# Kernel tuning notes

Measured on AMD Instinct MI355X. Metric: run time of the kernel, lower is better.

The kernel has to match this reference:

```python
import jax, jax.numpy as jnp
import numpy as np

PERIOD = 15          # hardcoded in the torch module's forward: STL(series, 15)
N_SEASONAL = 7       # statsmodels STL default seasonal smoother length
N_TREND = 29         # smallest odd >= 1.5*p/(1-1.5/7) = 28.64 -> 29 (statsmodels default)
N_LOWPASS = 17       # smallest odd > period (statsmodels default)
N_INNER = 2          # statsmodels: robust=False -> 2 inner iterations, 0 outer


def _loess_matrix(n, q, ts):
    """Dense linear operator for degree-1 LOESS smoothing of a length-n series
    evaluated at (possibly out-of-range) integer positions ts. Non-robust LOESS is
    linear in y, so smoothing == matmul with this constant matrix."""
    M = np.zeros((len(ts), n), dtype=np.float64)
    qq = min(q, n)
    for i, t in enumerate(ts):
        left = int(np.clip(t - (q - 1) // 2, 0, n - qq))
        right = left + qq - 1
        h = max(t - left, right - t)
        if q > n:
            h += (q - n) / 2.0
        xs = np.arange(left, right + 1, dtype=np.float64)
        w = np.clip(1.0 - (np.abs(xs - t) / h) ** 3, 0.0, None) ** 3  # tricube
        w = w / w.sum()
        xbar = (w * xs).sum()
        var = (w * (xs - xbar) ** 2).sum()
        a = w.copy()
        if var > 1e-12:  # degree-1 local linear fit; fall back to deg-0 if degenerate
            a = w * (1.0 + (t - xbar) * (xs - xbar) / var)
        M[i, left:right + 1] = a
    return M.astype(np.float32)


def _ma(x, k):
    """Moving average of window k along last axis (valid mode)."""
    cs = jnp.cumsum(x, axis=-1)
    cs = jnp.concatenate([jnp.zeros(x.shape[:-1] + (1,), x.dtype), cs], axis=-1)
    return (cs[..., k:] - cs[..., :-k]) / k


def setup_inputs() -> dict:
    key = jax.random.key(0)
    x = jax.random.normal(key, (128, 480, 256), dtype=jnp.float32)  # [B, T, C]
    return {"x": x}


def reference(x):
    B, T, Cc = x.shape
    p = PERIOD
    n_sub = T // p  # cycle-subseries length; T chosen divisible by period

    # Constant LOESS smoothing operators (numpy, baked in as jit constants)
    M_seas = jnp.asarray(_loess_matrix(n_sub, N_SEASONAL, np.arange(-1, n_sub + 1)))  # (n_sub+2, n_sub)
    M_lp = jnp.asarray(_loess_matrix(T, N_LOWPASS, np.arange(T)))                     # (T, T)
    M_trend = jnp.asarray(_loess_matrix(T, N_TREND, np.arange(T)))                    # (T, T)

    y = jnp.transpose(x, (0, 2, 1))  # [B, C, T]
    trend = jnp.zeros_like(y)
    seasonal = jnp.zeros_like(y)

    for _ in range(N_INNER):  # STL inner loop (Cleveland 1990, non-robust)
        # 1. detrend
        D = y - trend
        # 2. cycle-subseries LOESS smoothing, extended one period each side
        Dsub = D.reshape(B, Cc, n_sub, p)                      # subseries along axis 2
        Cext = jnp.einsum('sn,bcnp->bcsp', M_seas, Dsub)       # [B,C,n_sub+2,p]
        Cext = Cext.reshape(B, Cc, (n_sub + 2) * p)            # time order, length T+2p
        # 3. low-pass: MA(p) x2, MA(3), then LOESS(n_l)
        lp = _ma(_ma(_ma(Cext, p), p), 3)                      # length T
        L = jnp.einsum('tn,bcn->bct', M_lp, lp)
        # 4. seasonal = smoothed subseries (center T) minus low-pass
        seasonal = Cext[..., p:p + T] - L
        # 5+6. deseasonalize and trend LOESS
        trend = jnp.einsum('tn,bcn->bct', M_trend, y - seasonal)

    resid = y - seasonal - trend
    seas_plus_resid = jnp.transpose(seasonal + resid, (0, 2, 1))  # [B, T, C]
    trend_out = jnp.transpose(trend, (0, 2, 1))
    return (seas_plus_resid, trend_out)
```

## Files before the change

kernel.cpp:

```cpp
#include <hip/hip_runtime.h>
#include <hip/hip_bf16.h>
#include <stdint.h>

#define TLEN 480
#define NB 128
#define NC 256

typedef short bf16x8 __attribute__((ext_vector_type(8)));
typedef float f32x4 __attribute__((ext_vector_type(4)));
typedef unsigned int u32x4 __attribute__((ext_vector_type(4)));
typedef unsigned short u16;
typedef unsigned int u32;

__device__ inline u16 f2bf(float f) {
    union { float f; uint32_t u; } v; v.f = f;
    uint32_t u = v.u;
    return (u16)((u + 0x7fffu + ((u >> 16) & 1u)) >> 16);
}

__device__ inline u32 pack2bf(float lo, float hi) {
    return __builtin_amdgcn_perm(__float_as_uint(hi), __float_as_uint(lo), 0x07060302u);
}

template<int N, int Q>
__device__ __forceinline__ int loess_wT(int t, float* out) {
    int left = t - (Q - 1) / 2;
    if (left < 0) left = 0;
    if (left > N - Q) left = N - Q;
    int right = left + Q - 1;
    int h = (t - left) > (right - t) ? (t - left) : (right - t);
    double w[Q];
    double wsum = 0.0;
    #pragma unroll
    for (int i = 0; i < Q; ++i) {
        double dist = fabs((double)(left + i - t)) / (double)h;
        double u = 1.0 - dist * dist * dist;
        if (u < 0.0) u = 0.0;
        double wv = u * u * u;
        w[i] = wv; wsum += wv;
    }
    #pragma unroll
    for (int i = 0; i < Q; ++i) w[i] /= wsum;
    double xbar = 0.0;
    #pragma unroll
    for (int i = 0; i < Q; ++i) xbar += w[i] * (double)(left + i);
    double var = 0.0;
    #pragma unroll
    for (int i = 0; i < Q; ++i) { double d = (double)(left + i) - xbar; var += w[i] * d * d; }
    if (var > 1e-12) {
        double tb = (double)t - xbar;
        #pragma unroll
        for (int i = 0; i < Q; ++i) {
            double d = (double)(left + i) - xbar;
            out[i] = (float)(w[i] * (1.0 + tb * d / var));
        }
    } else {
        #pragma unroll
        for (int i = 0; i < Q; ++i) out[i] = (float)w[i];
    }
    return left;
}

__global__ void k_loess(float* Ms, float* w3, float* MlpC, float* MtC) {
    int gid = blockIdx.x * 256 + threadIdx.x;
    if (gid < 34) {
        float wl[7];
        int left = loess_wT<32, 7>(gid - 1, wl);
        float* row = Ms + gid * 32;
        #pragma unroll
        for (int i = 0; i < 32; ++i) row[i] = 0.0f;
        #pragma unroll
        for (int i = 0; i < 7; ++i) row[left + i] = wl[i];
    } else if (gid < 514) {
        int t = gid - 34;
        float wl[17];
        loess_wT<TLEN, 17>(t, wl);
        #pragma unroll
        for (int i = 0; i < 17; ++i) MlpC[t * 17 + i] = wl[i];
    } else if (gid < 994) {
        int t = gid - 514;
        float wl[29];
        loess_wT<TLEN, 29>(t, wl);
        #pragma unroll
        for (int i = 0; i < 29; ++i) MtC[t * 29 + i] = wl[i];
    } else if (gid < 1025) {
        int d = gid - 994;
        int cnt = 0;
        for (int c = 0; c < 3; ++c)
            for (int a = 0; a < 15; ++a) {
                int b = d - a - c;
                if (b >= 0 && b < 15) cnt++;
            }
        w3[d] = (float)((double)cnt / 675.0);
    }
}

__global__ __launch_bounds__(256, 2)
void k_T(const float* __restrict__ x, u16* __restrict__ xT) {
    __shared__ u16 Xs[64 * 488];
    int b = blockIdx.x;
    int cz = blockIdx.y * 64;
    int tid = threadIdx.x;
    int wq = tid & 15, kkq = tid >> 4;
    const float* xp0 = x + (size_t)b * TLEN * NC + (size_t)(kkq * 4) * NC + cz + wq * 4;
    u32* l32 = (u32*)Xs;
    int lbase = (wq * 4) * 244 + kkq * 2;

    float4 ra[4], rb[4];
    #pragma unroll
    for (int q = 0; q < 4; ++q) ra[q] = *(const float4*)(xp0 + q * NC);
    #pragma unroll
    for (int p = 0; p < 8; ++p) {
        float4* cur = (p & 1) ? rb : ra;
        float4* nxt = (p & 1) ? ra : rb;
        if (p < 7) {
            if (p + 1 < 7 || kkq < 8) {
                const float* xp = xp0 + (size_t)(p + 1) * 64 * NC;
                #pragma unroll
                for (int q = 0; q < 4; ++q) nxt[q] = *(const float4*)(xp + q * NC);
            }
        }
        if (p < 7 || kkq < 8) {
            const float* fl = (const float*)cur;
            int o = lbase + p * 32;
            #pragma unroll
            for (int cc = 0; cc < 4; ++cc) {
                uint2 w;
                w.x = pack2bf(fl[0 * 4 + cc], fl[1 * 4 + cc]);
                w.y = pack2bf(fl[2 * 4 + cc], fl[3 * 4 + cc]);
                *(uint2*)(l32 + o + cc * 244) = w;
            }
        }
    }
    __syncthreads();

    u16* dst = xT + ((size_t)b * NC + cz) * TLEN;
    #pragma unroll
    for (int v = 0; v < 15; ++v) {
        int id = v * 256 + tid;
        int c = id / 60, j = id - c * 60;
        *(u32x4*)(dst + (size_t)c * TLEN + j * 8) = *(const u32x4*)&Xs[c * 488 + j * 8];
    }
}

__global__ void k_S(const float* __restrict__ Ms, const float* __restrict__ w3,
                    const float* __restrict__ MlpC, float* __restrict__ S) {
    int id = blockIdx.x * 256 + threadIdx.x;
    if (id >= TLEN * TLEN) return;
    int t = id / TLEN, u = id - t * TLEN;
    int nu = u / 15, ju = u - nu * 15;
    int slp = t - 8;
    if (slp < 0) slp = 0;
    if (slp > TLEN - 17) slp = TLEN - 17;
    float acc = 0.0f;
    for (int k = 0; k < 17; ++k) {
        int i = slp + k;
        int s_lo = (i - ju + 14) / 15;
        float g = 0.0f;
        #pragma unroll
        for (int ds = 0; ds < 3; ++ds) {
            int s = s_lo + ds;
            int d = s * 15 + ju - i;
            if (s >= 0 && s < 34 && d >= 0 && d <= 30)
                g += Ms[s * 32 + nu] * w3[d];
        }
        acc += MlpC[t * 17 + k] * g;
    }
    float val = -acc;
    if (t % 15 == ju) val += Ms[(1 + t / 15) * 32 + nu];
    S[id] = val;
}

__global__ void k_VU(const float* __restrict__ MtC, const float* __restrict__ S,
                     float* __restrict__ U, float* __restrict__ V) {
    int id = blockIdx.x * 256 + threadIdx.x;
    if (id >= TLEN * TLEN) return;
    int t = id / TLEN, u = id - t * TLEN;
    int st = t - 14;
    if (st < 0) st = 0;
    if (st > TLEN - 29) st = TLEN - 29;
    float acc = 0.0f;
    for (int k = 0; k < 29; ++k)
        acc += MtC[t * 29 + k] * S[(size_t)(st + k) * TLEN + u];
    float mt = (u >= st && u < st + 29) ? MtC[t * 29 + (u - st)] : 0.0f;
    V[id] = acc;
    U[id] = mt - acc;
}

__global__ void k_A(const float* __restrict__ U, const float* __restrict__ V,
                    u16* __restrict__ Abf) {
    __shared__ float Vs[16][17];
    __shared__ float Us[16][17];
    int tx = threadIdx.x, ty = threadIdx.y;
    int u = blockIdx.x * 16 + tx;
    int t = blockIdx.y * 16 + ty;
    float acc = 0.0f;
    for (int kt = 0; kt < 30; ++kt) {
        Vs[ty][tx] = V[(size_t)t * TLEN + kt * 16 + tx];
        Us[ty][tx] = U[(size_t)(kt * 16 + ty) * TLEN + u];
        __syncthreads();
        #pragma unroll
        for (int e = 0; e < 16; ++e) acc += Vs[ty][e] * Us[e][tx];
        __syncthreads();
    }
    Abf[(size_t)t * TLEN + u] = f2bf(U[(size_t)t * TLEN + u] + acc);
}

__global__ __launch_bounds__(256, 3)
void k_gemm(const u16* __restrict__ A, const u16* __restrict__ xT,
            const float* __restrict__ x,
            float* __restrict__ out0, float* __restrict__ out1) {
    __shared__ float T[96 * 68];
    int b = blockIdx.x;
    int t0 = blockIdx.y * 96;
    int cz = blockIdx.z * 64;
    int tid = threadIdx.x;
    int wave = tid >> 6, lane = tid & 63;
    int lane15 = lane & 15, quad = lane >> 4;
    int wc = wave & 1, wt = wave >> 1;

    const u16* ap0 = xT + ((size_t)b * NC + cz + wc * 32 + lane15) * TLEN + quad * 8;
    const u16* bp0 = A + (size_t)(t0 + wt * 48 + lane15) * TLEN + quad * 8;

    f32x4 acc[2][3] = {};
    bf16x8 acur[2], anxt[2], bcur[3], bnxt[3];
    acur[0] = *(const bf16x8*)ap0;
    acur[1] = *(const bf16x8*)(ap0 + 16 * TLEN);
    #pragma unroll
    for (int j = 0; j < 3; ++j) bcur[j] = *(const bf16x8*)(bp0 + (size_t)j * 16 * TLEN);

    #pragma unroll
    for (int s = 0; s < 15; ++s) {
        bf16x8* ac = (s & 1) ? anxt : acur;
        bf16x8* an = (s & 1) ? acur : anxt;
        bf16x8* bc = (s & 1) ? bnxt : bcur;
        bf16x8* bn = (s & 1) ? bcur : bnxt;
        if (s < 14) {
            int k = (s + 1) * 32;
            an[0] = *(const bf16x8*)(ap0 + k);
            an[1] = *(const bf16x8*)(ap0 + 16 * TLEN + k);
            #pragma unroll
            for (int j = 0; j < 3; ++j)
                bn[j] = *(const bf16x8*)(bp0 + (size_t)j * 16 * TLEN + k);
        }
        #pragma unroll
        for (int j = 0; j < 3; ++j) {
            acc[0][j] = __builtin_amdgcn_mfma_f32_16x16x32_bf16(ac[0], bc[j], acc[0][j], 0, 0, 0);
            acc[1][j] = __builtin_amdgcn_mfma_f32_16x16x32_bf16(ac[1], bc[j], acc[1][j], 0, 0, 0);
        }
    }

    #pragma unroll
    for (int i = 0; i < 2; ++i)
        #pragma unroll
        for (int j = 0; j < 3; ++j) {
            int tl = wt * 48 + j * 16 + lane15;
            int cl = wc * 32 + i * 16 + quad * 4;
            *(f32x4*)&T[tl * 68 + cl] = acc[i][j];
        }
    __syncthreads();

    #pragma unroll
    for (int v = 0; v < 6; ++v) {
        int id = v * 256 + tid;
        int tl = id >> 4, c4 = (id & 15) * 4;
        size_t gb = ((size_t)b * TLEN + t0 + tl) * NC + cz + c4;
        f32x4 tv = *(const f32x4*)&T[tl * 68 + c4];
        f32x4 xv = *(const f32x4*)(x + gb);
        __builtin_nontemporal_store(tv, (f32x4*)(out1 + gb));
        __builtin_nontemporal_store(xv - tv, (f32x4*)(out0 + gb));
    }
}

extern "C" void kernel_launch(void* const* d_in, const int* in_sizes, int n_in,
                              void* d_out, int out_size, void* d_ws, size_t ws_size,
                              hipStream_t stream) {
    const float* x = (const float*)d_in[0];
    float* out0 = (float*)d_out;
    float* out1 = (float*)d_out + (size_t)NB * TLEN * NC;

    char* ws = (char*)d_ws;
    size_t oMs  = 0;
    size_t oW3  = oMs + 4352;
    size_t oLpC = oW3 + 128;
    size_t oMtC = oLpC + 32640;
    size_t oS   = oMtC + 55680;
    size_t oU   = oS + 921600;
    size_t oV   = oU + 921600;
    size_t oA   = oV + 921600;
    size_t oXT  = oA + 460800;

    float* Ms   = (float*)(ws + oMs);
    float* w3   = (float*)(ws + oW3);
    float* MlpC = (float*)(ws + oLpC);
    float* MtC  = (float*)(ws + oMtC);
    float* S    = (float*)(ws + oS);
    float* U    = (float*)(ws + oU);
    float* V    = (float*)(ws + oV);
    u16*   Abf  = (u16*)(ws + oA);
    u16*   xT   = (u16*)(ws + oXT);

    k_loess<<<5, 256, 0, stream>>>(Ms, w3, MlpC, MtC);
    k_T<<<dim3(NB, 4), 256, 0, stream>>>(x, xT);
    k_S<<<900, 256, 0, stream>>>(Ms, w3, MlpC, S);
    k_VU<<<900, 256, 0, stream>>>(MtC, S, U, V);
    k_A<<<dim3(30, 30), dim3(16, 16), 0, stream>>>(U, V, Abf);
    k_gemm<<<dim3(NB, 5, 4), 256, 0, stream>>>(Abf, xT, x, out0, out1);
}
```

Measured before the change: 277.8 us.

## Fuse U/V construction and A product into one shared-memory kernel

Replaces the separate k_VU and k_A kernels with a single k_VUA kernel. Each block computes its U column slice and V row chunks on the fly in shared memory from S and builds the combined operator tile directly, so the full U and V matrices never go through global memory. Each block recomputes V and U parts redundantly and uses a large LDS footprint (~62KB), which may limit occupancy. It also raises k_gemm's launch bounds occupancy hint from 3 to 4.

```diff
diff --git a/kernel.cpp b/kernel.cpp
--- a/kernel.cpp
+++ b/kernel.cpp
@@ -171,42 +171,78 @@
     S[id] = val;
 }
 
-__global__ void k_VU(const float* __restrict__ MtC, const float* __restrict__ S,
-                     float* __restrict__ U, float* __restrict__ V) {
-    int id = blockIdx.x * 256 + threadIdx.x;
-    if (id >= TLEN * TLEN) return;
-    int t = id / TLEN, u = id - t * TLEN;
-    int st = t - 14;
-    if (st < 0) st = 0;
-    if (st > TLEN - 29) st = TLEN - 29;
-    float acc = 0.0f;
-    for (int k = 0; k < 29; ++k)
-        acc += MtC[t * 29 + k] * S[(size_t)(st + k) * TLEN + u];
-    float mt = (u >= st && u < st + 29) ? MtC[t * 29 + (u - st)] : 0.0f;
-    V[id] = acc;
-    U[id] = mt - acc;
-}
-
-__global__ void k_A(const float* __restrict__ U, const float* __restrict__ V,
-                    u16* __restrict__ Abf) {
-    __shared__ float Vs[16][17];
-    __shared__ float Us[16][17];
-    int tx = threadIdx.x, ty = threadIdx.y;
-    int u = blockIdx.x * 16 + tx;
-    int t = blockIdx.y * 16 + ty;
-    float acc = 0.0f;
-    for (int kt = 0; kt < 30; ++kt) {
-        Vs[ty][tx] = V[(size_t)t * TLEN + kt * 16 + tx];
-        Us[ty][tx] = U[(size_t)(kt * 16 + ty) * TLEN + u];
+__global__ __launch_bounds__(256)
+void k_VUA(const float* __restrict__ MtC, const float* __restrict__ S,
+           u16* __restrict__ Abf) {
+    __shared__ float Uc[480 * 16];
+    __shared__ float Sbuf[7680];
+    __shared__ float MtCt[16 * 29];
+    int tid = threadIdx.x;
+    int u0 = blockIdx.x * 16, t0 = blockIdx.y * 16;
+    int tu = tid & 15, tk = tid >> 4;
+
+    for (int i = tid; i < 16 * 29; i += 256) MtCt[i] = MtC[(t0 + i / 29) * 29 + i % 29];
+
+    float* Su = Sbuf;
+    #pragma unroll
+    for (int it = 0; it < 30; ++it) {
+        int k = tk + 16 * it;
+        Su[k * 16 + tu] = S[(size_t)k * TLEN + u0 + tu];
+    }
+    __syncthreads();
+
+    #pragma unroll 2
+    for (int it = 0; it < 30; ++it) {
+        int k = tk + 16 * it;
+        int st = k - 14; if (st < 0) st = 0; if (st > TLEN - 29) st = TLEN - 29;
+        float acc = 0.0f;
+        for (int j = 0; j < 29; ++j) acc += MtC[k * 29 + j] * Su[(st + j) * 16 + tu];
+        int u = u0 + tu;
+        float mt = (u >= st && u < st + 29) ? MtC[k * 29 + (u - st)] : 0.0f;
+        Uc[k * 16 + tu] = mt - acc;
+    }
+    __syncthreads();
+
+    float* Schunk = Sbuf;
+    float* Vch = Sbuf + 44 * 121;
+    int rlo = t0 - 14; if (rlo < 0) rlo = 0; if (rlo > TLEN - 44) rlo = TLEN - 44;
+    float a = 0.0f;
+    for (int k0 = 0; k0 < 480; k0 += 120) {
+        for (int idx = tid; idx < 44 * 120; idx += 256) {
+            int r = idx / 120, c = idx - r * 120;
+            Schunk[r * 121 + c] = S[(size_t)(rlo + r) * TLEN + k0 + c];
+        }
         __syncthreads();
-        #pragma unroll
-        for (int e = 0; e < 16; ++e) acc += Vs[ty][e] * Us[e][tx];
+        {
+            int tt = tid & 15, cg = tid >> 4;
+            int st = t0 + tt - 14; if (st < 0) st = 0; if (st > TLEN - 29) st = TLEN - 29;
+            int ro = st - rlo;
+            #pragma unroll
+            for (int i = 0; i < 8; ++i) {
+                int c = cg + 16 * i;
+                if (c < 120) {
+                    float v = 0.0f;
+                    #pragma unroll
+                    for (int j = 0; j < 29; ++j)
+                        v += MtCt[tt * 29 + j] * Schunk[(ro + j) * 121 + c];
+                    Vch[tt * 121 + c] = v;
+                }
+            }
+        }
         __syncthreads();
-    }
-    Abf[(size_t)t * TLEN + u] = f2bf(U[(size_t)t * TLEN + u] + acc);
-}
-
-__global__ __launch_bounds__(256, 3)
+        {
+            int tt = tid >> 4;
+            for (int c = 0; c < 120; ++c)
+                a += Vch[tt * 121 + c] * Uc[(k0 + c) * 16 + tu];
+        }
+        __syncthreads();
+    }
+    int tt = tid >> 4;
+    a += Uc[(t0 + tt) * 16 + tu];
+    Abf[(size_t)(t0 + tt) * TLEN + u0 + tu] = f2bf(a);
+}
+
+__global__ __launch_bounds__(256, 4)
 void k_gemm(const u16* __restrict__ A, const u16* __restrict__ xT,
             const float* __restrict__ x,
             float* __restrict__ out0, float* __restrict__ out1) {
@@ -285,9 +321,7 @@
     size_t oLpC = oW3 + 128;
     size_t oMtC = oLpC + 32640;
     size_t oS   = oMtC + 55680;
-    size_t oU   = oS + 921600;
-    size_t oV   = oU + 921600;
-    size_t oA   = oV + 921600;
+    size_t oA   = oS + 921600;
     size_t oXT  = oA + 460800;
 
     float* Ms   = (float*)(ws + oMs);
@@ -295,15 +329,12 @@
     float* MlpC = (float*)(ws + oLpC);
     float* MtC  = (float*)(ws + oMtC);
     float* S    = (float*)(ws + oS);
-    float* U    = (float*)(ws + oU);
-    float* V    = (float*)(ws + oV);
     u16*   Abf  = (u16*)(ws + oA);
     u16*   xT   = (u16*)(ws + oXT);
 
     k_loess<<<5, 256, 0, stream>>>(Ms, w3, MlpC, MtC);
     k_T<<<dim3(NB, 4), 256, 0, stream>>>(x, xT);
     k_S<<<900, 256, 0, stream>>>(Ms, w3, MlpC, S);
-    k_VU<<<900, 256, 0, stream>>>(MtC, S, U, V);
-    k_A<<<dim3(30, 30), dim3(16, 16), 0, stream>>>(U, V, Abf);
+    k_VUA<<<dim3(30, 30), 256, 0, stream>>>(MtC, S, Abf);
     k_gemm<<<dim3(NB, 5, 4), 256, 0, stream>>>(Abf, xT, x, out0, out1);
 }
```

After: 338.5 us. 21.9% more time.
